# Kernel tuning notes

Measured on AMD Instinct MI355X. Metric: run time of the kernel, lower is better.

The kernel has to match this reference:

```python
import jax, jax.numpy as jnp
import numpy as np

N_ATOMS = 100000
N_PAIRS = 6400000
BOX_L = 100.0  # Angstrom, cubic box


def setup_inputs() -> dict:
    key = jax.random.key(0)
    k1, k2, k3, k4, k5 = jax.random.split(key, 5)
    coords = jax.random.uniform(k1, (N_ATOMS, 3), dtype=jnp.float32) * BOX_L
    # build pairs with guaranteed i != j (avoids dr == 0 -> inf/nan)
    i = jax.random.randint(k2, (N_PAIRS,), 0, N_ATOMS)
    off = jax.random.randint(k3, (N_PAIRS,), 1, N_ATOMS)
    pairs = jnp.stack([i, (i + off) % N_ATOMS], axis=1)
    box = jnp.eye(3, dtype=jnp.float32) * BOX_L
    sigma = jax.random.uniform(k4, (N_ATOMS,), dtype=jnp.float32) * 1.0 + 2.5
    epsilon = jax.random.uniform(k5, (N_ATOMS,), dtype=jnp.float32) * 0.4 + 0.05
    return {"coords": coords, "pairs": pairs, "box": box,
            "sigma": sigma, "epsilon": epsilon, "cutoff": 12}


def reference(coords, pairs, box, sigma, epsilon, cutoff):
    i, j = pairs[:, 0], pairs[:, 1]
    dr_vecs = coords[i] - coords[j]                 # [P,3] gather + diff
    box_inv = jnp.linalg.inv(box)                   # [3,3]
    ds = dr_vecs @ box_inv                          # fractional coords
    ds = ds - jnp.floor(ds + 0.5)                   # PBC minimum-image fold
    dr_pbc = ds @ box                               # back to cartesian
    dr = jnp.linalg.norm(dr_pbc, axis=1)            # [P]
    mask = dr <= cutoff
    sigma_ij = (sigma[i] + sigma[j]) * 0.5          # Lorentz mixing
    epsilon_ij = jnp.sqrt(epsilon[i] * epsilon[j])  # Berthelot mixing
    tmp = (sigma_ij / dr) ** 6
    ene = 4.0 * epsilon_ij * tmp * (tmp - 1.0)
    return jnp.sum(ene * mask)
```

## Files before the change

kernel.cpp:

```cpp
#include <hip/hip_runtime.h>
#include <hip/hip_fp16.h>

#define BLOCK 256
#define MAIN_BLOCKS_NOF 4096
#define FBLOCK 1024
#define FGRID 512

__global__ void lj_prep_kernel(const float* __restrict__ coords,
                               const float* __restrict__ sigma,
                               const float* __restrict__ eps,
                               const float* __restrict__ box,
                               float4* __restrict__ table,
                               unsigned char* __restrict__ cellg,
                               int n_atoms) {
    int i = blockIdx.x * blockDim.x + threadIdx.x;
    if (i >= n_atoms) return;
    float x = coords[3 * i + 0];
    float y = coords[3 * i + 1];
    float z = coords[3 * i + 2];
    float s  = sigma[i];
    float se = sqrtf(eps[i]);
    unsigned pack = (unsigned)__half_as_ushort(__float2half(s)) |
                    ((unsigned)__half_as_ushort(__float2half(se)) << 16);
    table[i] = make_float4(x, y, z, __uint_as_float(pack));

    float L0 = box[0], L1 = box[4], L2 = box[8];
    int cx = min((int)(x * (8.0f / L0)), 7); cx = max(cx, 0);
    int cy = min((int)(y * (8.0f / L1)), 7); cy = max(cy, 0);
    int cz = min((int)(z * (4.0f / L2)), 3); cz = max(cz, 0);
    cellg[i] = (unsigned char)(cx | (cy << 3) | (cz << 6));
}

__device__ __forceinline__ float lj_energy(float4 pi, float4 pj,
                                           float L0, float L1, float L2,
                                           float b0, float b1, float b2,
                                           float c2) {
    float dx = pi.x - pj.x;
    float dy = pi.y - pj.y;
    float dz = pi.z - pj.z;
    float sx = dx * b0; sx -= floorf(sx + 0.5f); dx = sx * L0;
    float sy = dy * b1; sy -= floorf(sy + 0.5f); dy = sy * L1;
    float sz = dz * b2; sz -= floorf(sz + 0.5f); dz = sz * L2;
    float r2 = dx * dx + dy * dy + dz * dz;

    unsigned packi = __float_as_uint(pi.w);
    unsigned packj = __float_as_uint(pj.w);
    float si  = __half2float(__ushort_as_half((unsigned short)(packi & 0xffffu)));
    float sj  = __half2float(__ushort_as_half((unsigned short)(packj & 0xffffu)));
    float sei = __half2float(__ushort_as_half((unsigned short)(packi >> 16)));
    float sej = __half2float(__ushort_as_half((unsigned short)(packj >> 16)));

    float sij   = (si + sj) * 0.5f;
    float epsij = sei * sej;
    float ratio = (sij * sij) / r2;
    float t     = ratio * ratio * ratio;
    float e     = 4.0f * epsij * t * (t - 1.0f);
    return (r2 <= c2) ? e : 0.0f;
}

__global__ __launch_bounds__(FBLOCK) void lj_main_filtered(
        const int2* __restrict__ pairs,
        const float4* __restrict__ table,
        const unsigned char* __restrict__ cellg,
        const float* __restrict__ box,
        const int* __restrict__ cutoff,
        float* __restrict__ out,
        int n_atoms, int n_pairs) {
    extern __shared__ unsigned char cellLds[];

    int n16 = n_atoms >> 4;
    const uint4* src = (const uint4*)cellg;
    uint4* dst = (uint4*)cellLds;
    for (int k = threadIdx.x; k < n16; k += blockDim.x) dst[k] = src[k];
    for (int k = (n16 << 4) + threadIdx.x; k < n_atoms; k += blockDim.x)
        cellLds[k] = cellg[k];
    __syncthreads();

    const float L0 = box[0], L1 = box[4], L2 = box[8];
    const float b0 = 1.0f / L0, b1 = 1.0f / L1, b2 = 1.0f / L2;
    const float c  = (float)cutoff[0];
    const float c2 = c * c;
    const bool use_filter = (c <= L0 * 0.125f) && (c <= L1 * 0.125f) &&
                            (c <= L2 * 0.25f);

    float acc = 0.0f;
    int tid = blockIdx.x * blockDim.x + threadIdx.x;
    int stride = gridDim.x * blockDim.x;
    for (int p = tid; p < n_pairs; p += stride) {
        int2 ij = pairs[p];
        unsigned ci = cellLds[ij.x];
        unsigned cj = cellLds[ij.y];
        unsigned dcx = (ci - cj) & 7u;
        unsigned dcy = ((ci >> 3) - (cj >> 3)) & 7u;
        unsigned dcz = ((ci >> 6) - (cj >> 6)) & 3u;
        bool near = (dcx <= 1u || dcx == 7u) &&
                    (dcy <= 1u || dcy == 7u) &&
                    (dcz <= 1u || dcz == 3u);
        if (near || !use_filter) {
            float4 pi = table[ij.x];
            float4 pj = table[ij.y];
            acc += lj_energy(pi, pj, L0, L1, L2, b0, b1, b2, c2);
        }
    }

    for (int off = 32; off > 0; off >>= 1)
        acc += __shfl_down(acc, off, 64);

    __shared__ float wsum[FBLOCK / 64];
    int lane = threadIdx.x & 63;
    int wid  = threadIdx.x >> 6;
    if (lane == 0) wsum[wid] = acc;
    __syncthreads();
    if (threadIdx.x == 0) {
        float s = 0.0f;
        for (int w = 0; w < FBLOCK / 64; w++) s += wsum[w];
        atomicAdd(out, s);
    }
}

__global__ __launch_bounds__(BLOCK) void lj_main_kernel(
        const int2* __restrict__ pairs,
        const float4* __restrict__ table,
        const float* __restrict__ box,
        const int* __restrict__ cutoff,
        float* __restrict__ out,
        int n_pairs) {
    const float L0 = box[0], L1 = box[4], L2 = box[8];
    const float b0 = 1.0f / L0, b1 = 1.0f / L1, b2 = 1.0f / L2;
    const float c  = (float)cutoff[0];
    const float c2 = c * c;

    float acc = 0.0f;
    int tid = blockIdx.x * blockDim.x + threadIdx.x;
    int stride = gridDim.x * blockDim.x;
    for (int p = tid; p < n_pairs; p += stride) {
        int2 ij = pairs[p];
        float4 pi = table[ij.x];
        float4 pj = table[ij.y];
        acc += lj_energy(pi, pj, L0, L1, L2, b0, b1, b2, c2);
    }
    for (int off = 32; off > 0; off >>= 1)
        acc += __shfl_down(acc, off, 64);
    __shared__ float wsum[BLOCK / 64];
    int lane = threadIdx.x & 63;
    int wid  = threadIdx.x >> 6;
    if (lane == 0) wsum[wid] = acc;
    __syncthreads();
    if (threadIdx.x == 0) {
        float s = 0.0f;
        for (int w = 0; w < BLOCK / 64; w++) s += wsum[w];
        atomicAdd(out, s);
    }
}

extern "C" void kernel_launch(void* const* d_in, const int* in_sizes, int n_in,
                              void* d_out, int out_size, void* d_ws, size_t ws_size,
                              hipStream_t stream) {
    const float* coords = (const float*)d_in[0];
    const int2*  pairs  = (const int2*)d_in[1];
    const float* box    = (const float*)d_in[2];
    const float* sigma  = (const float*)d_in[3];
    const float* eps    = (const float*)d_in[4];
    const int*   cutoff = (const int*)d_in[5];
    int n_atoms = in_sizes[0] / 3;
    int n_pairs = in_sizes[1] / 2;
    float* out = (float*)d_out;

    size_t table_bytes = ((size_t)n_atoms * sizeof(float4) + 255) & ~(size_t)255;
    size_t cell_bytes  = (size_t)n_atoms;
    float4* table = (float4*)d_ws;
    unsigned char* cellg = (unsigned char*)d_ws + table_bytes;

    hipMemsetAsync(d_out, 0, sizeof(float), stream);

    bool can_filter = (ws_size >= table_bytes + cell_bytes) &&
                      (n_atoms <= 160000);

    if (can_filter) {
        lj_prep_kernel<<<(n_atoms + 255) / 256, 256, 0, stream>>>(
            coords, sigma, eps, box, table, cellg, n_atoms);
        static bool attr_set = false;
        if (!attr_set) {
            hipFuncSetAttribute((const void*)lj_main_filtered,
                                hipFuncAttributeMaxDynamicSharedMemorySize,
                                n_atoms);
            attr_set = true;
        }
        lj_main_filtered<<<FGRID, FBLOCK, n_atoms, stream>>>(
            pairs, table, cellg, box, cutoff, out, n_atoms, n_pairs);
    } else {
        lj_prep_kernel<<<(n_atoms + 255) / 256, 256, 0, stream>>>(
            coords, sigma, eps, box, table, cellg, n_atoms);
        lj_main_kernel<<<MAIN_BLOCKS_NOF, BLOCK, 0, stream>>>(
            pairs, table, box, cutoff, out, n_pairs);
    }
}
```

Baseline: 118.1 us.

## Compact near pairs into per-wave LDS queues before gathering table entries

The filtered kernel now uses a wave ballot to compact the pairs that pass the cell filter into a per-wave LDS queue, and evaluates LJ energy only when 64 entries are ready, so no lanes sit idle on divergent gathers. It also software-prefetches the next pair index and halves the grid to 256 blocks. The cost is extra LDS traffic, a larger shared-memory footprint and fewer blocks. Occupancy may drop, since each block already holds about 100KB of cell data.

Measured after the change: 107.2 us. 1.1x faster.

```diff
diff --git a/kernel.cpp b/kernel.cpp
--- a/kernel.cpp
+++ b/kernel.cpp
@@ -4,7 +4,9 @@
 #define BLOCK 256
 #define MAIN_BLOCKS_NOF 4096
 #define FBLOCK 1024
-#define FGRID 512
+#define FGRID 256
+#define NWAVES (FBLOCK / 64)
+#define QCAP 128
 
 __global__ void lj_prep_kernel(const float* __restrict__ coords,
                                const float* __restrict__ sigma,
@@ -65,8 +67,12 @@
         const float* __restrict__ box,
         const int* __restrict__ cutoff,
         float* __restrict__ out,
-        int n_atoms, int n_pairs) {
-    extern __shared__ unsigned char cellLds[];
+        int n_atoms, int n_pairs, int qoff) {
+    extern __shared__ unsigned char lds[];
+    unsigned char* cellLds = lds;
+    int lane = threadIdx.x & 63;
+    int wid  = threadIdx.x >> 6;
+    int2* queue = (int2*)(lds + qoff) + wid * QCAP;
 
     int n16 = n_atoms >> 4;
     const uint4* src = (const uint4*)cellg;
@@ -84,36 +90,64 @@
                             (c <= L2 * 0.25f);
 
     float acc = 0.0f;
-    int tid = blockIdx.x * blockDim.x + threadIdx.x;
-    int stride = gridDim.x * blockDim.x;
-    for (int p = tid; p < n_pairs; p += stride) {
-        int2 ij = pairs[p];
+    int qcount = 0;
+
+    long base = ((long)blockIdx.x * NWAVES + wid) * 64;
+    long step = (long)gridDim.x * NWAVES * 64;
+
+    bool v = (base + lane) < n_pairs;
+    int2 ij = v ? pairs[base + lane] : make_int2(0, 0);
+
+    while (base < n_pairs) {
+        long nbase = base + step;
+        bool vn = (nbase + lane) < n_pairs;
+        int2 ijn = vn ? pairs[nbase + lane] : make_int2(0, 0);
+
         unsigned ci = cellLds[ij.x];
         unsigned cj = cellLds[ij.y];
         unsigned dcx = (ci - cj) & 7u;
         unsigned dcy = ((ci >> 3) - (cj >> 3)) & 7u;
         unsigned dcz = ((ci >> 6) - (cj >> 6)) & 3u;
-        bool near = (dcx <= 1u || dcx == 7u) &&
-                    (dcy <= 1u || dcy == 7u) &&
-                    (dcz <= 1u || dcz == 3u);
-        if (near || !use_filter) {
-            float4 pi = table[ij.x];
-            float4 pj = table[ij.y];
+        bool near = v && (!use_filter ||
+                          ((dcx <= 1u || dcx == 7u) &&
+                           (dcy <= 1u || dcy == 7u) &&
+                           (dcz <= 1u || dcz == 3u)));
+
+        unsigned long long bal = __ballot(near);
+        int pos = (int)__popcll(bal & ((1ull << lane) - 1ull));
+        if (near) queue[qcount + pos] = ij;
+        qcount += (int)__popcll(bal);
+
+        if (qcount >= 64) {
+            int2 e = queue[lane];
+            float4 pi = table[e.x];
+            float4 pj = table[e.y];
             acc += lj_energy(pi, pj, L0, L1, L2, b0, b1, b2, c2);
+            qcount -= 64;
+            if (lane < qcount) {
+                int2 t = queue[64 + lane];
+                queue[lane] = t;
+            }
         }
+
+        base = nbase; ij = ijn; v = vn;
+    }
+    if (lane < qcount) {
+        int2 e = queue[lane];
+        float4 pi = table[e.x];
+        float4 pj = table[e.y];
+        acc += lj_energy(pi, pj, L0, L1, L2, b0, b1, b2, c2);
     }
 
     for (int off = 32; off > 0; off >>= 1)
         acc += __shfl_down(acc, off, 64);
 
-    __shared__ float wsum[FBLOCK / 64];
-    int lane = threadIdx.x & 63;
-    int wid  = threadIdx.x >> 6;
+    __shared__ float wsum[NWAVES];
     if (lane == 0) wsum[wid] = acc;
     __syncthreads();
     if (threadIdx.x == 0) {
         float s = 0.0f;
-        for (int w = 0; w < FBLOCK / 64; w++) s += wsum[w];
+        for (int w = 0; w < NWAVES; w++) s += wsum[w];
         atomicAdd(out, s);
     }
 }
@@ -171,26 +205,27 @@
     float4* table = (float4*)d_ws;
     unsigned char* cellg = (unsigned char*)d_ws + table_bytes;
 
+    int qoff = (n_atoms + 15) & ~15;
+    int shmem = qoff + NWAVES * QCAP * (int)sizeof(int2);
+
     hipMemsetAsync(d_out, 0, sizeof(float), stream);
+    lj_prep_kernel<<<(n_atoms + 255) / 256, 256, 0, stream>>>(
+        coords, sigma, eps, box, table, cellg, n_atoms);
 
     bool can_filter = (ws_size >= table_bytes + cell_bytes) &&
-                      (n_atoms <= 160000);
+                      (shmem <= 160 * 1024 - 1024);
 
     if (can_filter) {
-        lj_prep_kernel<<<(n_atoms + 255) / 256, 256, 0, stream>>>(
-            coords, sigma, eps, box, table, cellg, n_atoms);
         static bool attr_set = false;
         if (!attr_set) {
             hipFuncSetAttribute((const void*)lj_main_filtered,
                                 hipFuncAttributeMaxDynamicSharedMemorySize,
-                                n_atoms);
+                                shmem);
             attr_set = true;
         }
-        lj_main_filtered<<<FGRID, FBLOCK, n_atoms, stream>>>(
-            pairs, table, cellg, box, cutoff, out, n_atoms, n_pairs);
+        lj_main_filtered<<<FGRID, FBLOCK, shmem, stream>>>(
+            pairs, table, cellg, box, cutoff, out, n_atoms, n_pairs, qoff);
     } else {
-        lj_prep_kernel<<<(n_atoms + 255) / 256, 256, 0, stream>>>(
-            coords, sigma, eps, box, table, cellg, n_atoms);
         lj_main_kernel<<<MAIN_BLOCKS_NOF, BLOCK, 0, stream>>>(
             pairs, table, box, cutoff, out, n_pairs);
     }
```
